# Optimization experiments

Hardware: AMD Instinct MI355X
Metric: run time of the kernel (lower is better)

The kernel has to match this reference:

```python
import jax, jax.numpy as jnp
from jax import lax
import numpy as np

B, T, IN, H, OUT = 8192, 512, 8, 64, 1


def setup_inputs() -> dict:
    key = jax.random.key(0)
    ks = jax.random.split(key, 7)
    s_ih = 1.0 / np.sqrt(H)
    # PyTorch LSTM param layout: gates stacked as [i, f, g, o] along dim 0
    W_ih = jax.random.uniform(ks[0], (4 * H, IN), jnp.float32, -s_ih, s_ih)
    W_hh = jax.random.uniform(ks[1], (4 * H, H), jnp.float32, -s_ih, s_ih)
    b_ih = jax.random.uniform(ks[2], (4 * H,), jnp.float32, -s_ih, s_ih)
    b_hh = jax.random.uniform(ks[3], (4 * H,), jnp.float32, -s_ih, s_ih)
    W_fc = jax.random.uniform(ks[4], (OUT, H), jnp.float32, -s_ih, s_ih)
    b_fc = jax.random.uniform(ks[5], (OUT,), jnp.float32, -s_ih, s_ih)
    x = jax.random.normal(ks[6], (B, T, IN), jnp.float32)
    return {"x": x, "W_ih": W_ih, "W_hh": W_hh, "b_ih": b_ih,
            "b_hh": b_hh, "W_fc": W_fc, "b_fc": b_fc}


def _lstm_last_h(x, W_ih, W_hh, b_ih, b_hh):
    # x: [B, T, IN] -> last hidden state [B, H]
    Bn = x.shape[0]
    Hn = W_hh.shape[1]
    b = b_ih + b_hh  # [4H]

    def step(carry, xt):
        h, c = carry  # [B, H] each
        gates = xt @ W_ih.T + h @ W_hh.T + b  # [B, 4H]
        i, f, g, o = jnp.split(gates, 4, axis=-1)
        i = jax.nn.sigmoid(i)
        f = jax.nn.sigmoid(f)
        g = jnp.tanh(g)
        o = jax.nn.sigmoid(o)
        c = f * c + i * g
        h = o * jnp.tanh(c)
        return (h, c), None

    h0 = jnp.zeros((Bn, Hn), x.dtype)
    c0 = jnp.zeros((Bn, Hn), x.dtype)
    (hT, _), _ = lax.scan(step, (h0, c0), jnp.swapaxes(x, 0, 1))  # scan over T
    return hT


def reference(x, W_ih, W_hh, b_ih, b_hh, W_fc, b_fc):
    hT = _lstm_last_h(x, W_ih, W_hh, b_ih, b_hh)  # [B, H]
    return hT @ W_fc.T + b_fc  # [B, OUT]
```

## Files before the change

### kernel.cpp

```cpp
#include <hip/hip_runtime.h>


typedef _Float16 f16_t;
typedef _Float16 half8 __attribute__((ext_vector_type(8)));
typedef __fp16 fp16x2 __attribute__((ext_vector_type(2)));
typedef float floatx2 __attribute__((ext_vector_type(2)));
typedef float floatx4 __attribute__((ext_vector_type(4)));

#define Bn 8192
#define Tn 512
#define INn 8
#define Hn 64
#define BT 16
#define CHUNK 16
#define NCHUNK (Tn / CHUNK)
#define HSTRIDE 72
#define XTSTRIDE 136

__device__ __forceinline__ floatx2 act_pair(float zi0, float zi1,
                                            float zf0, float zf1,
                                            float zg0, float zg1,
                                            float zo0, float zo1,
                                            floatx2& chat) {
  const floatx2 one  = {1.f, 1.f};
  const float  K2   = 2.8853900817779268f;
  const floatx2 K2v  = {K2, K2};
  const floatx2 mK2v = {-K2, -K2};
  const floatx2 clmp = {126.f, 126.f};
  floatx2 A = {__builtin_amdgcn_exp2f(zi0), __builtin_amdgcn_exp2f(zi1)};
  floatx2 G = {__builtin_amdgcn_exp2f(zg0), __builtin_amdgcn_exp2f(zg1)};
  floatx2 F = {__builtin_amdgcn_exp2f(zf0), __builtin_amdgcn_exp2f(zf1)};
  floatx2 O = {__builtin_amdgcn_exp2f(zo0), __builtin_amdgcn_exp2f(zo1)};
  floatx2 PA  = A + one;
  floatx2 PG  = G + one;
  floatx2 PF  = F + one;
  floatx2 PAG = PA * PG;
  floatx2 num = __builtin_elementwise_fma(G, K2v, mK2v) * PF;
  floatx2 s   = __builtin_elementwise_fma(chat, PAG, num);
  floatx2 P3  = PF * PAG;
  floatx2 R   = {__builtin_amdgcn_rcpf(P3.x), __builtin_amdgcn_rcpf(P3.y)};
  chat = __builtin_elementwise_min(s * R, clmp);
  floatx2 C2 = {__builtin_amdgcn_exp2f(chat.x), __builtin_amdgcn_exp2f(chat.y)};
  floatx2 P4 = (O + one) * (C2 + one);
  floatx2 Rh = {__builtin_amdgcn_rcpf(P4.x), __builtin_amdgcn_rcpf(P4.y)};
  return (C2 - one) * Rh;
}

__global__ __launch_bounds__(256, 2)
void lstm_fused(const float* __restrict__ xg,
                const float* __restrict__ W_ih,
                const float* __restrict__ W_hh,
                const float* __restrict__ b_ih,
                const float* __restrict__ b_hh,
                const float* __restrict__ W_fc,
                const float* __restrict__ b_fc,
                float* __restrict__ out)
{
  __shared__ alignas(16) f16_t hbuf[2][BT][HSTRIDE];
  __shared__ alignas(16) f16_t xlds[2][CHUNK][XTSTRIDE];

  const int tid   = threadIdx.x;
  const int wv    = tid >> 6;
  const int lane  = tid & 63;
  const int n     = lane & 15;
  const int q     = lane >> 4;
  const int bbase = blockIdx.x * BT;

  const float LOG2E = 1.4426950408889634f;

  half8 bf[4][3];
  #pragma unroll
  for (int g = 0; g < 4; ++g) {
    const float sc = (g == 2) ? (2.f * LOG2E) : (-LOG2E);
    const int C = g * 64 + wv * 16 + n;
    #pragma unroll
    for (int c = 0; c < 3; ++c) {
      half8 v;
      #pragma unroll
      for (int j = 0; j < 8; ++j) {
        const int k = c * 32 + q * 8 + j;
        float w = 0.f;
        if (k < Hn)            w = W_hh[C * Hn + k] * sc;
        else if (k < Hn + INn) w = W_ih[C * INn + (k - Hn)] * sc;
        v[j] = (f16_t)w;
      }
      bf[g][c] = v;
    }
  }

  const int u = wv * 16 + n;
  const float pb_i = -(b_ih[u]       + b_hh[u])       * LOG2E;
  const float pb_f = -(b_ih[64 + u]  + b_hh[64 + u])  * LOG2E;
  const float pb_g =  (b_ih[128 + u] + b_hh[128 + u]) * (2.f * LOG2E);
  const float pb_o = -(b_ih[192 + u] + b_hh[192 + u]) * LOG2E;
  const floatx4 bi  = {pb_i, pb_i, pb_i, pb_i};
  const floatx4 bfv = {pb_f, pb_f, pb_f, pb_f};
  const floatx4 bg  = {pb_g, pb_g, pb_g, pb_g};
  const floatx4 bo  = {pb_o, pb_o, pb_o, pb_o};

  for (int i = tid; i < BT * HSTRIDE; i += 256) ((f16_t*)hbuf[0])[i] = (f16_t)0.f;

  const int row_s = tid >> 4;
  const int tt_s  = tid & 15;
  const float* xps = xg + ((size_t)(bbase + row_s) * Tn + tt_s) * INn;

  float4 pa = *(const float4*)(xps);
  float4 pb2 = *(const float4*)(xps + 4);

  floatx2 chat01 = {0.f, 0.f};
  floatx2 chat23 = {0.f, 0.f};

  for (int ch = 0; ch < NCHUNK; ++ch) {
    union { half8 v; fp16x2 h2[4]; } P;
    P.h2[0] = __builtin_amdgcn_cvt_pkrtz(pa.x, pa.y);
    P.h2[1] = __builtin_amdgcn_cvt_pkrtz(pa.z, pa.w);
    P.h2[2] = __builtin_amdgcn_cvt_pkrtz(pb2.x, pb2.y);
    P.h2[3] = __builtin_amdgcn_cvt_pkrtz(pb2.z, pb2.w);
    *(half8*)&xlds[ch & 1][tt_s][row_s * 8] = P.v;
    __syncthreads();

    const int chn = (ch + 1 < NCHUNK) ? (ch + 1) : 0;
    pa  = *(const float4*)(xps + (size_t)chn * CHUNK * INn);
    pb2 = *(const float4*)(xps + (size_t)chn * CHUNK * INn + 4);

    #pragma unroll
    for (int tt = 0; tt < CHUNK; ++tt) {
      const int p  = tt & 1;
      const int pn = p ^ 1;

      const half8 a0 = *(const half8*)&hbuf[p][n][q * 8];
      const half8 a1 = *(const half8*)&hbuf[p][n][32 + q * 8];
      const half8 a2 = *(const half8*)&xlds[ch & 1][tt][n * 8];

      floatx4 ai = __builtin_amdgcn_mfma_f32_16x16x32_f16(a0, bf[0][0], bi, 0, 0, 0);
      ai = __builtin_amdgcn_mfma_f32_16x16x32_f16(a1, bf[0][1], ai, 0, 0, 0);
      ai = __builtin_amdgcn_mfma_f32_16x16x32_f16(a2, bf[0][2], ai, 0, 0, 0);
      floatx4 af = __builtin_amdgcn_mfma_f32_16x16x32_f16(a0, bf[1][0], bfv, 0, 0, 0);
      af = __builtin_amdgcn_mfma_f32_16x16x32_f16(a1, bf[1][1], af, 0, 0, 0);
      af = __builtin_amdgcn_mfma_f32_16x16x32_f16(a2, bf[1][2], af, 0, 0, 0);
      floatx4 ag = __builtin_amdgcn_mfma_f32_16x16x32_f16(a0, bf[2][0], bg, 0, 0, 0);
      ag = __builtin_amdgcn_mfma_f32_16x16x32_f16(a1, bf[2][1], ag, 0, 0, 0);
      ag = __builtin_amdgcn_mfma_f32_16x16x32_f16(a2, bf[2][2], ag, 0, 0, 0);
      floatx4 ao = __builtin_amdgcn_mfma_f32_16x16x32_f16(a0, bf[3][0], bo, 0, 0, 0);
      ao = __builtin_amdgcn_mfma_f32_16x16x32_f16(a1, bf[3][1], ao, 0, 0, 0);
      ao = __builtin_amdgcn_mfma_f32_16x16x32_f16(a2, bf[3][2], ao, 0, 0, 0);

      const floatx2 h01 = act_pair(ai[0], ai[1], af[0], af[1],
                                   ag[0], ag[1], ao[0], ao[1], chat01);
      const floatx2 h23 = act_pair(ai[2], ai[3], af[2], af[3],
                                   ag[2], ag[3], ao[2], ao[3], chat23);

      hbuf[pn][q * 4 + 0][u] = (f16_t)h01.x;
      hbuf[pn][q * 4 + 1][u] = (f16_t)h01.y;
      hbuf[pn][q * 4 + 2][u] = (f16_t)h23.x;
      hbuf[pn][q * 4 + 3][u] = (f16_t)h23.y;

      __syncthreads();
    }
  }

  if (tid < 64) {
    const int b = lane & 15;
    const int part = lane >> 4;
    float s = 0.f;
    #pragma unroll
    for (int k = 0; k < 16; ++k) {
      const int uu = part * 16 + k;
      s = __builtin_fmaf((float)hbuf[0][b][uu], W_fc[uu], s);
    }
    s += __shfl_down(s, 32);
    s += __shfl_down(s, 16);
    if (lane < 16) out[bbase + b] = s + b_fc[0];
  }
}

extern "C" void kernel_launch(void* const* d_in, const int* in_sizes, int n_in,
                              void* d_out, int out_size, void* d_ws, size_t ws_size,
                              hipStream_t stream) {
  const float* x    = (const float*)d_in[0];
  const float* W_ih = (const float*)d_in[1];
  const float* W_hh = (const float*)d_in[2];
  const float* b_ih = (const float*)d_in[3];
  const float* b_hh = (const float*)d_in[4];
  const float* W_fc = (const float*)d_in[5];
  const float* b_fc = (const float*)d_in[6];
  float* out = (float*)d_out;
  dim3 grid(Bn / BT), block(256);
  hipLaunchKernelGGL(lstm_fused, grid, block, 0, stream,
                     x, W_ih, W_hh, b_ih, b_hh, W_fc, b_fc, out);
}
```

Baseline: 448.5 us.

## Split LSTM gates across twice as many waves with swizzle exchange

New measurement: 478.0 us. 1.07x slower.

```diff
diff --git a/kernel.cpp b/kernel.cpp
--- a/kernel.cpp
+++ b/kernel.cpp
@@ -3,6 +3,7 @@
 
 typedef _Float16 f16_t;
 typedef _Float16 half8 __attribute__((ext_vector_type(8)));
+typedef _Float16 half4 __attribute__((ext_vector_type(4)));
 typedef __fp16 fp16x2 __attribute__((ext_vector_type(2)));
 typedef float floatx2 __attribute__((ext_vector_type(2)));
 typedef float floatx4 __attribute__((ext_vector_type(4)));
@@ -46,7 +47,7 @@
   return (C2 - one) * Rh;
 }
 
-__global__ __launch_bounds__(256, 2)
+__global__ __launch_bounds__(512, 4)
 void lstm_fused(const float* __restrict__ xg,
                 const float* __restrict__ W_ih,
                 const float* __restrict__ W_hh,
@@ -64,64 +65,64 @@
   const int lane  = tid & 63;
   const int n     = lane & 15;
   const int q     = lane >> 4;
+  const int j     = lane & 7;
+  const int s     = (lane >> 3) & 1;
   const int bbase = blockIdx.x * BT;
 
   const float LOG2E = 1.4426950408889634f;
 
-  half8 bf[4][3];
+  const int u = 8 * wv + j;
+  const int gate0 = s ? 1 : 0;
+  const int gate1 = s ? 3 : 2;
+  half8 bt[2][3];
   #pragma unroll
-  for (int g = 0; g < 4; ++g) {
-    const float sc = (g == 2) ? (2.f * LOG2E) : (-LOG2E);
-    const int C = g * 64 + wv * 16 + n;
+  for (int tl = 0; tl < 2; ++tl) {
+    const int gate = tl ? gate1 : gate0;
+    const float sc = (gate == 2) ? (2.f * LOG2E) : (-LOG2E);
+    const int Crow = gate * 64 + u;
     #pragma unroll
-    for (int c = 0; c < 3; ++c) {
+    for (int kc = 0; kc < 3; ++kc) {
       half8 v;
       #pragma unroll
-      for (int j = 0; j < 8; ++j) {
-        const int k = c * 32 + q * 8 + j;
+      for (int e = 0; e < 8; ++e) {
+        const int k = kc * 32 + q * 8 + e;
         float w = 0.f;
-        if (k < Hn)            w = W_hh[C * Hn + k] * sc;
-        else if (k < Hn + INn) w = W_ih[C * INn + (k - Hn)] * sc;
-        v[j] = (f16_t)w;
+        if (k < Hn)            w = W_hh[Crow * Hn + k] * sc;
+        else if (k < Hn + INn) w = W_ih[Crow * INn + (k - Hn)] * sc;
+        v[e] = (f16_t)w;
       }
-      bf[g][c] = v;
+      bt[tl][kc] = v;
     }
   }
 
-  const int u = wv * 16 + n;
-  const float pb_i = -(b_ih[u]       + b_hh[u])       * LOG2E;
-  const float pb_f = -(b_ih[64 + u]  + b_hh[64 + u])  * LOG2E;
-  const float pb_g =  (b_ih[128 + u] + b_hh[128 + u]) * (2.f * LOG2E);
-  const float pb_o = -(b_ih[192 + u] + b_hh[192 + u]) * LOG2E;
-  const floatx4 bi  = {pb_i, pb_i, pb_i, pb_i};
-  const floatx4 bfv = {pb_f, pb_f, pb_f, pb_f};
-  const floatx4 bg  = {pb_g, pb_g, pb_g, pb_g};
-  const floatx4 bo  = {pb_o, pb_o, pb_o, pb_o};
-
-  for (int i = tid; i < BT * HSTRIDE; i += 256) ((f16_t*)hbuf[0])[i] = (f16_t)0.f;
-
-  const int row_s = tid >> 4;
-  const int tt_s  = tid & 15;
-  const float* xps = xg + ((size_t)(bbase + row_s) * Tn + tt_s) * INn;
+  const float sc0 = (gate0 == 2) ? (2.f * LOG2E) : (-LOG2E);
+  const float sc1 = (gate1 == 2) ? (2.f * LOG2E) : (-LOG2E);
+  const float pb0 = (b_ih[gate0 * 64 + u] + b_hh[gate0 * 64 + u]) * sc0;
+  const float pb1 = (b_ih[gate1 * 64 + u] + b_hh[gate1 * 64 + u]) * sc1;
+  const floatx4 bias0 = {pb0, pb0, pb0, pb0};
+  const floatx4 bias1 = {pb1, pb1, pb1, pb1};
+
+  for (int i = tid; i < BT * HSTRIDE; i += 512) ((f16_t*)hbuf[0])[i] = (f16_t)0.f;
+
+  const int row_s = tid >> 5;
+  const int tt_s  = (tid >> 1) & 15;
+  const int hf_s  = tid & 1;
+  const float* xps = xg + ((size_t)(bbase + row_s) * Tn + tt_s) * INn + hf_s * 4;
 
   float4 pa = *(const float4*)(xps);
-  float4 pb2 = *(const float4*)(xps + 4);
-
-  floatx2 chat01 = {0.f, 0.f};
-  floatx2 chat23 = {0.f, 0.f};
+
+  floatx2 chat = {0.f, 0.f};
+  const int ra = 4 * q + 2 * s;
 
   for (int ch = 0; ch < NCHUNK; ++ch) {
-    union { half8 v; fp16x2 h2[4]; } P;
+    union { half4 v; fp16x2 h2[2]; } P;
     P.h2[0] = __builtin_amdgcn_cvt_pkrtz(pa.x, pa.y);
     P.h2[1] = __builtin_amdgcn_cvt_pkrtz(pa.z, pa.w);
-    P.h2[2] = __builtin_amdgcn_cvt_pkrtz(pb2.x, pb2.y);
-    P.h2[3] = __builtin_amdgcn_cvt_pkrtz(pb2.z, pb2.w);
-    *(half8*)&xlds[ch & 1][tt_s][row_s * 8] = P.v;
+    *(half4*)&xlds[ch & 1][tt_s][row_s * 8 + hf_s * 4] = P.v;
     __syncthreads();
 
     const int chn = (ch + 1 < NCHUNK) ? (ch + 1) : 0;
-    pa  = *(const float4*)(xps + (size_t)chn * CHUNK * INn);
-    pb2 = *(const float4*)(xps + (size_t)chn * CHUNK * INn + 4);
+    pa = *(const float4*)(xps + (size_t)chn * CHUNK * INn);
 
     #pragma unroll
     for (int tt = 0; tt < CHUNK; ++tt) {
@@ -132,28 +133,38 @@
       const half8 a1 = *(const half8*)&hbuf[p][n][32 + q * 8];
       const half8 a2 = *(const half8*)&xlds[ch & 1][tt][n * 8];
 
-      floatx4 ai = __builtin_amdgcn_mfma_f32_16x16x32_f16(a0, bf[0][0], bi, 0, 0, 0);
-      ai = __builtin_amdgcn_mfma_f32_16x16x32_f16(a1, bf[0][1], ai, 0, 0, 0);
-      ai = __builtin_amdgcn_mfma_f32_16x16x32_f16(a2, bf[0][2], ai, 0, 0, 0);
-      floatx4 af = __builtin_amdgcn_mfma_f32_16x16x32_f16(a0, bf[1][0], bfv, 0, 0, 0);
-      af = __builtin_amdgcn_mfma_f32_16x16x32_f16(a1, bf[1][1], af, 0, 0, 0);
-      af = __builtin_amdgcn_mfma_f32_16x16x32_f16(a2, bf[1][2], af, 0, 0, 0);
-      floatx4 ag = __builtin_amdgcn_mfma_f32_16x16x32_f16(a0, bf[2][0], bg, 0, 0, 0);
-      ag = __builtin_amdgcn_mfma_f32_16x16x32_f16(a1, bf[2][1], ag, 0, 0, 0);
-      ag = __builtin_amdgcn_mfma_f32_16x16x32_f16(a2, bf[2][2], ag, 0, 0, 0);
-      floatx4 ao = __builtin_amdgcn_mfma_f32_16x16x32_f16(a0, bf[3][0], bo, 0, 0, 0);
-      ao = __builtin_amdgcn_mfma_f32_16x16x32_f16(a1, bf[3][1], ao, 0, 0, 0);
-      ao = __builtin_amdgcn_mfma_f32_16x16x32_f16(a2, bf[3][2], ao, 0, 0, 0);
-
-      const floatx2 h01 = act_pair(ai[0], ai[1], af[0], af[1],
-                                   ag[0], ag[1], ao[0], ao[1], chat01);
-      const floatx2 h23 = act_pair(ai[2], ai[3], af[2], af[3],
-                                   ag[2], ag[3], ao[2], ao[3], chat23);
-
-      hbuf[pn][q * 4 + 0][u] = (f16_t)h01.x;
-      hbuf[pn][q * 4 + 1][u] = (f16_t)h01.y;
-      hbuf[pn][q * 4 + 2][u] = (f16_t)h23.x;
-      hbuf[pn][q * 4 + 3][u] = (f16_t)h23.y;
+      floatx4 acc0 = __builtin_amdgcn_mfma_f32_16x16x32_f16(a0, bt[0][0], bias0, 0, 0, 0);
+      acc0 = __builtin_amdgcn_mfma_f32_16x16x32_f16(a1, bt[0][1], acc0, 0, 0, 0);
+      acc0 = __builtin_amdgcn_mfma_f32_16x16x32_f16(a2, bt[0][2], acc0, 0, 0, 0);
+      floatx4 acc1 = __builtin_amdgcn_mfma_f32_16x16x32_f16(a0, bt[1][0], bias1, 0, 0, 0);
+      acc1 = __builtin_amdgcn_mfma_f32_16x16x32_f16(a1, bt[1][1], acc1, 0, 0, 0);
+      acc1 = __builtin_amdgcn_mfma_f32_16x16x32_f16(a2, bt[1][2], acc1, 0, 0, 0);
+
+      const float sendA = s ? acc0[0] : acc0[2];
+      const float sendB = s ? acc0[1] : acc0[3];
+      const float sendC = s ? acc1[0] : acc1[2];
+      const float sendD = s ? acc1[1] : acc1[3];
+      const float rA = __int_as_float(
+          __builtin_amdgcn_ds_swizzle(__float_as_int(sendA), 0x201F));
+      const float rB = __int_as_float(
+          __builtin_amdgcn_ds_swizzle(__float_as_int(sendB), 0x201F));
+      const float rC = __int_as_float(
+          __builtin_amdgcn_ds_swizzle(__float_as_int(sendC), 0x201F));
+      const float rD = __int_as_float(
+          __builtin_amdgcn_ds_swizzle(__float_as_int(sendD), 0x201F));
+      const float zi0 = s ? rA : acc0[0];
+      const float zi1 = s ? rB : acc0[1];
+      const float zf0 = s ? acc0[2] : rA;
+      const float zf1 = s ? acc0[3] : rB;
+      const float zg0 = s ? rC : acc1[0];
+      const float zg1 = s ? rD : acc1[1];
+      const float zo0 = s ? acc1[2] : rC;
+      const float zo1 = s ? acc1[3] : rD;
+
+      const floatx2 h = act_pair(zi0, zi1, zf0, zf1, zg0, zg1, zo0, zo1, chat);
+
+      hbuf[pn][ra + 0][u] = (f16_t)h.x;
+      hbuf[pn][ra + 1][u] = (f16_t)h.y;
 
       __syncthreads();
     }
@@ -162,15 +173,15 @@
   if (tid < 64) {
     const int b = lane & 15;
     const int part = lane >> 4;
-    float s = 0.f;
+    float acc = 0.f;
     #pragma unroll
     for (int k = 0; k < 16; ++k) {
       const int uu = part * 16 + k;
-      s = __builtin_fmaf((float)hbuf[0][b][uu], W_fc[uu], s);
+      acc = __builtin_fmaf((float)hbuf[0][b][uu], W_fc[uu], acc);
     }
-    s += __shfl_down(s, 32);
-    s += __shfl_down(s, 16);
-    if (lane < 16) out[bbase + b] = s + b_fc[0];
+    acc += __shfl_down(acc, 32);
+    acc += __shfl_down(acc, 16);
+    if (lane < 16) out[bbase + b] = acc + b_fc[0];
   }
 }
 
@@ -185,7 +196,7 @@
   const float* W_fc = (const float*)d_in[5];
   const float* b_fc = (const float*)d_in[6];
   float* out = (float*)d_out;
-  dim3 grid(Bn / BT), block(256);
+  dim3 grid(Bn / BT), block(512);
   hipLaunchKernelGGL(lstm_fused, grid, block, 0, stream,
                      x, W_ih, W_hh, b_ih, b_hh, W_fc, b_fc, out);
 }
```
